# Kernel tuning notes

Measured on AMD Instinct MI355X. Metric: run time of the kernel, lower is better.

## Reference

```python
import jax, jax.numpy as jnp
import numpy as np

HIDDEN = 1024
HEADS = 16
HEAD_DIM = HIDDEN // HEADS


def setup_inputs() -> dict:
    key = jax.random.key(0)
    ks = jax.random.split(key, 9)
    s = 1.0 / np.sqrt(HIDDEN)  # nn.Linear default init scale (uniform bound)
    def lin(kw, kb):
        W = jax.random.uniform(kw, (HIDDEN, HIDDEN), jnp.float32, -s, s)
        b = jax.random.uniform(kb, (HIDDEN,), jnp.float32, -s, s)
        return W, b
    Wq, bq = lin(ks[0], ks[1])
    Wk, bk = lin(ks[2], ks[3])
    Wv, bv = lin(ks[4], ks[5])
    Wo, bo = lin(ks[6], ks[7])
    x = jax.random.normal(ks[8], (2, 2048, HIDDEN), jnp.float32)
    return {"x": x, "Wq": Wq, "bq": bq, "Wk": Wk, "bk": bk,
            "Wv": Wv, "bv": bv, "Wo": Wo, "bo": bo}


def reference(x, Wq, bq, Wk, bk, Wv, bv, Wo, bo):
    B, S, _ = x.shape
    # projections (torch Linear: y = x @ W.T + b)
    def proj(W, b):
        y = jnp.einsum('bsh,oh->bso', x, W) + b
        return y.reshape(B, S, HEADS, HEAD_DIM)
    q = proj(Wq, bq)  # [B,S,H,D]
    k = proj(Wk, bk)
    v = proj(Wv, bv)
    scale = 1.0 / np.sqrt(HEAD_DIM)
    scores = jnp.einsum('bqhd,bkhd->bhqk', q, k) * scale  # [B,H,S,S]
    probs = jax.nn.softmax(scores, axis=-1)
    out = jnp.einsum('bhqk,bkhd->bqhd', probs, v).reshape(B, S, HIDDEN)
    return jnp.einsum('bsh,oh->bso', out, Wo) + bo
```

## Files before the change

### kernel.cpp

```cpp
#include <hip/hip_runtime.h>
#include <hip/hip_bf16.h>
#include <stdint.h>

#define HIDDEN 1024
#define SEQ 2048
#define BATCH 2
#define HEADS 16
#define HDIM 64
#define M_TOK (BATCH * SEQ)

using bf16_t = __bf16;
typedef __attribute__((ext_vector_type(8))) __bf16 bf16x8;
typedef __attribute__((ext_vector_type(4))) float f32x4;

__device__ __forceinline__ bf16_t tobf(float f) {
  uint32_t u = __builtin_bit_cast(uint32_t, f);
  u += 0x7FFFu + ((u >> 16) & 1u);
  uint16_t h = (uint16_t)(u >> 16);
  return __builtin_bit_cast(bf16_t, h);
}

__device__ __forceinline__ void async_cp16(const bf16_t* g, bf16_t* l) {
  __builtin_amdgcn_global_load_lds(
      (const __attribute__((address_space(1))) uint32_t*)g,
      (__attribute__((address_space(3))) uint32_t*)l, 16, 0, 0);
}

__global__ __launch_bounds__(256) void k_convert(const float* __restrict__ src,
                                                 bf16_t* __restrict__ dst, int n) {
  int i = (blockIdx.x * 256 + threadIdx.x) * 4;
  if (i >= n) return;
  float4 v = *(const float4*)(src + i);
  union { bf16_t b[4]; uint64_t u; } o;
  o.b[0] = tobf(v.x); o.b[1] = tobf(v.y); o.b[2] = tobf(v.z); o.b[3] = tobf(v.w);
  *(uint64_t*)(dst + i) = o.u;
}

__global__ __launch_bounds__(256) void k_convert4(
    const float* __restrict__ s0, const float* __restrict__ s1,
    const float* __restrict__ s2, const float* __restrict__ s3,
    bf16_t* __restrict__ d0, bf16_t* __restrict__ d1,
    bf16_t* __restrict__ d2, bf16_t* __restrict__ d3) {
  const int wsel = blockIdx.y;
  const float* src = (wsel == 0) ? s0 : (wsel == 1) ? s1 : (wsel == 2) ? s2 : s3;
  bf16_t* dst = (wsel == 0) ? d0 : (wsel == 1) ? d1 : (wsel == 2) ? d2 : d3;
  int i = (blockIdx.x * 256 + threadIdx.x) * 4;
  float4 v = *(const float4*)(src + i);
  union { bf16_t b[4]; uint64_t u; } o;
  o.b[0] = tobf(v.x); o.b[1] = tobf(v.y); o.b[2] = tobf(v.z); o.b[3] = tobf(v.w);
  *(uint64_t*)(dst + i) = o.u;
}

template <int MODE>
__device__ __forceinline__ void gemm_bt_body(const bf16_t* __restrict__ A,
                                             const bf16_t* __restrict__ Bw,
                                             const float* __restrict__ bias,
                                             void* __restrict__ dst,
                                             bf16_t* As, bf16_t* Bs) {
  constexpr int K = HIDDEN;
  const int tid = threadIdx.x;
  const int lane = tid & 63;
  const int w = tid >> 6;
  const int wr = w >> 1, wc = w & 1;
  const int lr = lane & 15, lg = lane >> 4;
  const int m0 = blockIdx.x * 128;
  const int n0 = blockIdx.y * 128;

  f32x4 acc[4][4];
#pragma unroll
  for (int i = 0; i < 4; ++i)
#pragma unroll
    for (int j = 0; j < 4; ++j) acc[i][j] = f32x4{0.f, 0.f, 0.f, 0.f};

  for (int k0 = 0; k0 < K; k0 += 32) {
#pragma unroll
    for (int i = 0; i < 2; ++i) {
      int c = w * 128 + i * 64 + lane;
      int row = c >> 2, kc = c & 3;
      async_cp16(A + (size_t)(m0 + row) * K + k0 + kc * 8, As + c * 8);
      async_cp16(Bw + (size_t)(n0 + row) * K + k0 + kc * 8, Bs + c * 8);
    }
    __syncthreads();
    bf16x8 af[4], bfr[4];
#pragma unroll
    for (int mi = 0; mi < 4; ++mi)
      af[mi] = *(const bf16x8*)(As + (wr * 64 + mi * 16 + lr) * 32 + lg * 8);
#pragma unroll
    for (int ni = 0; ni < 4; ++ni)
      bfr[ni] = *(const bf16x8*)(Bs + (wc * 64 + ni * 16 + lr) * 32 + lg * 8);
#pragma unroll
    for (int mi = 0; mi < 4; ++mi)
#pragma unroll
      for (int ni = 0; ni < 4; ++ni)
        acc[mi][ni] = __builtin_amdgcn_mfma_f32_16x16x32_bf16(af[mi], bfr[ni], acc[mi][ni], 0, 0, 0);
    __syncthreads();
  }

#pragma unroll
  for (int ni = 0; ni < 4; ++ni) {
    int col = n0 + wc * 64 + ni * 16 + lr;
    float bv = bias[col];
#pragma unroll
    for (int mi = 0; mi < 4; ++mi) {
#pragma unroll
      for (int r = 0; r < 4; ++r) {
        int m = m0 + wr * 64 + mi * 16 + lg * 4 + r;
        float v = acc[mi][ni][r] + bv;
        if (MODE == 0) {
          int b = m >> 11, s = m & (SEQ - 1);
          int h = col >> 6, d = col & 63;
          ((bf16_t*)dst)[(((size_t)(b * HEADS + h) * SEQ) + s) * HDIM + d] = tobf(v);
        } else {
          ((float*)dst)[(size_t)m * HIDDEN + col] = v;
        }
      }
    }
  }
}

__global__ __launch_bounds__(256) void k_gemm_qkv(
    const bf16_t* __restrict__ A,
    const bf16_t* __restrict__ Wqb, const bf16_t* __restrict__ Wkb,
    const bf16_t* __restrict__ Wvb,
    const float* __restrict__ bq, const float* __restrict__ bk,
    const float* __restrict__ bv,
    bf16_t* __restrict__ Qb, bf16_t* __restrict__ Kb, bf16_t* __restrict__ Vb) {
  __shared__ bf16_t As[128 * 32];
  __shared__ bf16_t Bs[128 * 32];
  const int z = blockIdx.z;
  const bf16_t* Bw = (z == 0) ? Wqb : (z == 1) ? Wkb : Wvb;
  const float* bias = (z == 0) ? bq : (z == 1) ? bk : bv;
  bf16_t* dst = (z == 0) ? Qb : (z == 1) ? Kb : Vb;
  gemm_bt_body<0>(A, Bw, bias, dst, As, Bs);
}

__global__ __launch_bounds__(256) void k_gemm_out(const bf16_t* __restrict__ A,
                                                  const bf16_t* __restrict__ Bw,
                                                  const float* __restrict__ bias,
                                                  float* __restrict__ dst) {
  __shared__ bf16_t As[128 * 32];
  __shared__ bf16_t Bs[128 * 32];
  gemm_bt_body<1>(A, Bw, bias, dst, As, Bs);
}

__global__ __launch_bounds__(256) void k_attn(const bf16_t* __restrict__ Q,
                                              const bf16_t* __restrict__ Kk,
                                              const bf16_t* __restrict__ V,
                                              bf16_t* __restrict__ AO) {
  __shared__ bf16_t Vt[64 * 64];
  __shared__ bf16_t Pl[4][16 * 64];
  const int tid = threadIdx.x;
  const int lane = tid & 63;
  const int w = tid >> 6;
  const int lr = lane & 15, lg = lane >> 4;
  const int bh = blockIdx.y;
  const int q0 = blockIdx.x * 64 + w * 16;
  const bf16_t* Qh = Q + (size_t)bh * SEQ * HDIM;
  const bf16_t* Kh = Kk + (size_t)bh * SEQ * HDIM;
  const bf16_t* Vh = V + (size_t)bh * SEQ * HDIM;

  const float qscale = 0.125f * 1.44269504088896f;
  bf16x8 aq[2];
#pragma unroll
  for (int dc = 0; dc < 2; ++dc) {
    bf16x8 t = *(const bf16x8*)(Qh + (size_t)(q0 + lr) * HDIM + dc * 32 + lg * 8);
#pragma unroll
    for (int j = 0; j < 8; ++j) t[j] = tobf((float)t[j] * qscale);
    aq[dc] = t;
  }

  float mrow[4], lsum[4];
  f32x4 acc[4];
#pragma unroll
  for (int r = 0; r < 4; ++r) { mrow[r] = -1e30f; lsum[r] = 0.f; }
#pragma unroll
  for (int fc = 0; fc < 4; ++fc) acc[fc] = f32x4{0.f, 0.f, 0.f, 0.f};

  for (int kt = 0; kt < SEQ / 64; ++kt) {
    const int kr0 = kt * 64;
    __syncthreads();
    {
      int k = tid >> 2, d0 = (tid & 3) * 16;
      const bf16_t* vp = Vh + (size_t)(kr0 + k) * HDIM + d0;
#pragma unroll
      for (int half = 0; half < 2; ++half) {
        bf16x8 vv = *(const bf16x8*)(vp + half * 8);
#pragma unroll
        for (int j = 0; j < 8; ++j) {
          int d = d0 + half * 8 + j;
          Vt[d * 64 + (((k >> 3) ^ (d & 7)) * 8) + (k & 7)] = vv[j];
        }
      }
    }
    __syncthreads();

    f32x4 sf[4];
#pragma unroll
    for (int fc = 0; fc < 4; ++fc) {
      f32x4 a = f32x4{0.f, 0.f, 0.f, 0.f};
      int kr = kr0 + fc * 16 + lr;
#pragma unroll
      for (int dc = 0; dc < 2; ++dc) {
        bf16x8 bk = *(const bf16x8*)(Kh + (size_t)kr * HDIM + dc * 32 + lg * 8);
        a = __builtin_amdgcn_mfma_f32_16x16x32_bf16(aq[dc], bk, a, 0, 0, 0);
      }
      sf[fc] = a;
    }

    float pv[4][4];
#pragma unroll
    for (int r = 0; r < 4; ++r) {
      float mx = fmaxf(fmaxf(sf[0][r], sf[1][r]), fmaxf(sf[2][r], sf[3][r]));
      mx = fmaxf(mx, __shfl_xor(mx, 1));
      mx = fmaxf(mx, __shfl_xor(mx, 2));
      mx = fmaxf(mx, __shfl_xor(mx, 4));
      mx = fmaxf(mx, __shfl_xor(mx, 8));
      float mn = fmaxf(mrow[r], mx);
      float sc = exp2f(mrow[r] - mn);
      mrow[r] = mn;
      float ts = 0.f;
#pragma unroll
      for (int fc = 0; fc < 4; ++fc) {
        float p = exp2f(sf[fc][r] - mn);
        pv[fc][r] = p;
        ts += p;
      }
      ts += __shfl_xor(ts, 1);
      ts += __shfl_xor(ts, 2);
      ts += __shfl_xor(ts, 4);
      ts += __shfl_xor(ts, 8);
      lsum[r] = lsum[r] * sc + ts;
#pragma unroll
      for (int fc = 0; fc < 4; ++fc) acc[fc][r] = acc[fc][r] * sc;
    }

#pragma unroll
    for (int fc = 0; fc < 4; ++fc) {
      int col = fc * 16 + lr;
#pragma unroll
      for (int r = 0; r < 4; ++r) {
        int row = lg * 4 + r;
        Pl[w][row * 64 + (((col >> 3) ^ (row & 7)) * 8) + (col & 7)] = tobf(pv[fc][r]);
      }
    }

    bf16x8 pa[2];
#pragma unroll
    for (int kc = 0; kc < 2; ++kc) {
      int swz = (kc * 4 + lg) ^ (lr & 7);
      pa[kc] = *(const bf16x8*)(&Pl[w][lr * 64 + swz * 8]);
    }
#pragma unroll
    for (int fc = 0; fc < 4; ++fc) {
      int d = fc * 16 + lr;
#pragma unroll
      for (int kc = 0; kc < 2; ++kc) {
        int swz = (kc * 4 + lg) ^ (d & 7);
        bf16x8 bv = *(const bf16x8*)(&Vt[d * 64 + swz * 8]);
        acc[fc] = __builtin_amdgcn_mfma_f32_16x16x32_bf16(pa[kc], bv, acc[fc], 0, 0, 0);
      }
    }
  }

  const int b = bh >> 4, h = bh & 15;
#pragma unroll
  for (int fc = 0; fc < 4; ++fc) {
#pragma unroll
    for (int r = 0; r < 4; ++r) {
      int srow = q0 + lg * 4 + r;
      float o = acc[fc][r] / lsum[r];
      AO[((size_t)(b * SEQ + srow)) * HIDDEN + h * HDIM + fc * 16 + lr] = tobf(o);
    }
  }
}

extern "C" void kernel_launch(void* const* d_in, const int* in_sizes, int n_in,
                              void* d_out, int out_size, void* d_ws, size_t ws_size,
                              hipStream_t stream) {
  const float* x  = (const float*)d_in[0];
  const float* Wq = (const float*)d_in[1];
  const float* bq = (const float*)d_in[2];
  const float* Wk = (const float*)d_in[3];
  const float* bk = (const float*)d_in[4];
  const float* Wv = (const float*)d_in[5];
  const float* bv = (const float*)d_in[6];
  const float* Wo = (const float*)d_in[7];
  const float* bo = (const float*)d_in[8];

  char* ws = (char*)d_ws;
  const size_t XB = (size_t)M_TOK * HIDDEN * 2;
  const size_t WB = (size_t)HIDDEN * HIDDEN * 2;
  bf16_t* xb  = (bf16_t*)(ws);
  bf16_t* Wqb = (bf16_t*)(ws + XB);
  bf16_t* Wkb = (bf16_t*)(ws + XB + 1 * WB);
  bf16_t* Wvb = (bf16_t*)(ws + XB + 2 * WB);
  bf16_t* Wob = (bf16_t*)(ws + XB + 3 * WB);
  bf16_t* Qb  = (bf16_t*)(ws + XB + 4 * WB);
  bf16_t* Kb  = (bf16_t*)(ws + 2 * XB + 4 * WB);
  bf16_t* Vb  = (bf16_t*)(ws + 3 * XB + 4 * WB);
  bf16_t* AOb = (bf16_t*)(ws + 4 * XB + 4 * WB);

  k_convert<<<(M_TOK * HIDDEN) / 1024, 256, 0, stream>>>(x, xb, M_TOK * HIDDEN);
  k_convert4<<<dim3((HIDDEN * HIDDEN) / 1024, 4), 256, 0, stream>>>(
      Wq, Wk, Wv, Wo, Wqb, Wkb, Wvb, Wob);

  dim3 gg(M_TOK / 128, HIDDEN / 128);
  k_gemm_qkv<<<dim3(M_TOK / 128, HIDDEN / 128, 3), 256, 0, stream>>>(
      xb, Wqb, Wkb, Wvb, bq, bk, bv, Qb, Kb, Vb);

  k_attn<<<dim3(SEQ / 64, BATCH * HEADS), 256, 0, stream>>>(Qb, Kb, Vb, AOb);

  k_gemm_out<<<gg, 256, 0, stream>>>(AOb, Wob, bo, (float*)d_out);
}
```

Measured before the change: 231.5 us.

## Use lazy softmax rescaling, MFMA row sums, and MFMA priority hints in attention

Replaces the per-tile max shuffle reduction and rescale with a wave-uniform check that skips rescaling unless some row's new max exceeds the running max by more than a threshold of 8 in log2 units. The row-sum shuffle reduction is replaced by two extra MFMAs of P against a ones vector, accumulated alongside the output. s_setprio hints raise the wave's priority around the MFMA sections. This removes many cross-lane shuffles and exp operations per tile. The trade-off is that unnormalised P values can reach up to 2^8 before rounding to bf16, and the row sums now come from the bf16-rounded P.

Result: faster. 196.1 us (-15.3%).

```diff
diff --git a/kernel.cpp b/kernel.cpp
--- a/kernel.cpp
+++ b/kernel.cpp
@@ -169,10 +169,15 @@
     aq[dc] = t;
   }
 
-  float mrow[4], lsum[4];
+  bf16x8 vone;
+#pragma unroll
+  for (int j = 0; j < 8; ++j) vone[j] = tobf(1.0f);
+
+  float mrow[4];
   f32x4 acc[4];
-#pragma unroll
-  for (int r = 0; r < 4; ++r) { mrow[r] = -1e30f; lsum[r] = 0.f; }
+  f32x4 accd = f32x4{0.f, 0.f, 0.f, 0.f};
+#pragma unroll
+  for (int r = 0; r < 4; ++r) mrow[r] = -1e30f;
 #pragma unroll
   for (int fc = 0; fc < 4; ++fc) acc[fc] = f32x4{0.f, 0.f, 0.f, 0.f};
 
@@ -195,6 +200,7 @@
     __syncthreads();
 
     f32x4 sf[4];
+    __builtin_amdgcn_s_setprio(1);
 #pragma unroll
     for (int fc = 0; fc < 4; ++fc) {
       f32x4 a = f32x4{0.f, 0.f, 0.f, 0.f};
@@ -206,33 +212,35 @@
       }
       sf[fc] = a;
     }
-
+    __builtin_amdgcn_s_setprio(0);
+
+    float pmax[4];
+#pragma unroll
+    for (int r = 0; r < 4; ++r)
+      pmax[r] = fmaxf(fmaxf(sf[0][r], sf[1][r]), fmaxf(sf[2][r], sf[3][r]));
+    int ok = (pmax[0] <= mrow[0] + 8.f) && (pmax[1] <= mrow[1] + 8.f) &&
+             (pmax[2] <= mrow[2] + 8.f) && (pmax[3] <= mrow[3] + 8.f);
+    if (!__all(ok)) {
+#pragma unroll
+      for (int r = 0; r < 4; ++r) {
+        float mx = pmax[r];
+        mx = fmaxf(mx, __shfl_xor(mx, 1));
+        mx = fmaxf(mx, __shfl_xor(mx, 2));
+        mx = fmaxf(mx, __shfl_xor(mx, 4));
+        mx = fmaxf(mx, __shfl_xor(mx, 8));
+        float mn = fmaxf(mrow[r], mx);
+        float sc = exp2f(mrow[r] - mn);
+        mrow[r] = mn;
+        accd[r] *= sc;
+#pragma unroll
+        for (int fc = 0; fc < 4; ++fc) acc[fc][r] *= sc;
+      }
+    }
     float pv[4][4];
 #pragma unroll
-    for (int r = 0; r < 4; ++r) {
-      float mx = fmaxf(fmaxf(sf[0][r], sf[1][r]), fmaxf(sf[2][r], sf[3][r]));
-      mx = fmaxf(mx, __shfl_xor(mx, 1));
-      mx = fmaxf(mx, __shfl_xor(mx, 2));
-      mx = fmaxf(mx, __shfl_xor(mx, 4));
-      mx = fmaxf(mx, __shfl_xor(mx, 8));
-      float mn = fmaxf(mrow[r], mx);
-      float sc = exp2f(mrow[r] - mn);
-      mrow[r] = mn;
-      float ts = 0.f;
-#pragma unroll
-      for (int fc = 0; fc < 4; ++fc) {
-        float p = exp2f(sf[fc][r] - mn);
-        pv[fc][r] = p;
-        ts += p;
-      }
-      ts += __shfl_xor(ts, 1);
-      ts += __shfl_xor(ts, 2);
-      ts += __shfl_xor(ts, 4);
-      ts += __shfl_xor(ts, 8);
-      lsum[r] = lsum[r] * sc + ts;
-#pragma unroll
-      for (int fc = 0; fc < 4; ++fc) acc[fc][r] = acc[fc][r] * sc;
-    }
+    for (int r = 0; r < 4; ++r)
+#pragma unroll
+      for (int fc = 0; fc < 4; ++fc) pv[fc][r] = exp2f(sf[fc][r] - mrow[r]);
 
 #pragma unroll
     for (int fc = 0; fc < 4; ++fc) {
@@ -250,6 +258,7 @@
       int swz = (kc * 4 + lg) ^ (lr & 7);
       pa[kc] = *(const bf16x8*)(&Pl[w][lr * 64 + swz * 8]);
     }
+    __builtin_amdgcn_s_setprio(1);
 #pragma unroll
     for (int fc = 0; fc < 4; ++fc) {
       int d = fc * 16 + lr;
@@ -260,6 +269,9 @@
         acc[fc] = __builtin_amdgcn_mfma_f32_16x16x32_bf16(pa[kc], bv, acc[fc], 0, 0, 0);
       }
     }
+    accd = __builtin_amdgcn_mfma_f32_16x16x32_bf16(pa[0], vone, accd, 0, 0, 0);
+    accd = __builtin_amdgcn_mfma_f32_16x16x32_bf16(pa[1], vone, accd, 0, 0, 0);
+    __builtin_amdgcn_s_setprio(0);
   }
 
   const int b = bh >> 4, h = bh & 15;
@@ -268,7 +280,7 @@
 #pragma unroll
     for (int r = 0; r < 4; ++r) {
       int srow = q0 + lg * 4 + r;
-      float o = acc[fc][r] / lsum[r];
+      float o = acc[fc][r] / accd[r];
       AO[((size_t)(b * SEQ + srow)) * HIDDEN + h * HDIM + fc * 16 + lr] = tobf(o);
     }
   }
```
